# Optimization experiments

Hardware: AMD Instinct MI355X
Metric: run time of the kernel (lower is better)

## Reference

```python
import jax, jax.numpy as jnp
import numpy as np

B, S, E, H = 4, 8192, 1024, 16
D = E // H  # head_dim = 64


def setup_inputs() -> dict:
    key = jax.random.key(0)
    ks = jax.random.split(key, 9)
    s = 0.02
    return {
        "x": jax.random.normal(ks[0], (B, S, E), dtype=jnp.float32),
        "Wq": jax.random.normal(ks[1], (D, E), dtype=jnp.float32) * s,
        "bq": jax.random.normal(ks[2], (D,), dtype=jnp.float32) * s,
        "Wk": jax.random.normal(ks[3], (D, E), dtype=jnp.float32) * s,
        "bk": jax.random.normal(ks[4], (D,), dtype=jnp.float32) * s,
        "Wv": jax.random.normal(ks[5], (D, E), dtype=jnp.float32) * s,
        "bv": jax.random.normal(ks[6], (D,), dtype=jnp.float32) * s,
        "Wo": jax.random.normal(ks[7], (E, E), dtype=jnp.float32) * s,
        "bo": jax.random.normal(ks[8], (E,), dtype=jnp.float32) * s,
    }


def reference(x, Wq, bq, Wk, bk, Wv, bv, Wo, bo):
    b, s, e = x.shape
    d = Wq.shape[0]          # head_dim (projections map embed_dim -> head_dim)
    h = e // d               # num_heads
    # torch Linear: y = x @ W.T + b ; projected shape [B, S, d]
    # view(B, -1, h, d) on [B, S, d] => effective seq S' = S // h (faithful to source)
    def split_heads(t):
        return t.reshape(b, -1, h, d).transpose(0, 2, 1, 3)  # [B, H, S', D]
    q = split_heads(x @ Wq.T + bq)
    k = split_heads(x @ Wk.T + bk)
    v = split_heads(x @ Wv.T + bv)
    scores = jnp.einsum('bhqd,bhkd->bhqk', q, k) / np.sqrt(d).astype(jnp.float32)
    attn = jax.nn.softmax(scores, axis=-1)  # dropout=0.0 => identity
    ctx = jnp.einsum('bhqk,bhkd->bhqd', attn, v)
    ctx = ctx.transpose(0, 2, 1, 3).reshape(b, -1, e)  # [B, S', E]
    return ctx @ Wo.T + bo
```

## Files before the change

### kernel.cpp

```cpp
#include <hip/hip_runtime.h>
#include <hip/hip_bf16.h>


typedef unsigned short u16;
typedef __attribute__((ext_vector_type(8))) short short8;
typedef __attribute__((ext_vector_type(4))) float f32x4;

__device__ inline u16 f2bf(float f) {
    union { float f; unsigned u; } v; v.f = f;
    unsigned u = v.u;
    return (u16)((u + 0x7fffu + ((u >> 16) & 1u)) >> 16);
}
__device__ inline unsigned pack_bf2(float a, float b) {
    union { __hip_bfloat162 h; unsigned u; } v;
    v.h = __float22bfloat162_rn(float2{a, b});
    return v.u;
}
__device__ __forceinline__ void gld16(void* lds, const void* gptr) {
    __builtin_amdgcn_global_load_lds(
        (const __attribute__((address_space(1))) unsigned int*)gptr,
        (__attribute__((address_space(3))) unsigned int*)lds,
        16, 0, 0);
}

__global__ __launch_bounds__(256) void convw(
    const float* __restrict__ Wq, const float* __restrict__ bq,
    const float* __restrict__ Wk, const float* __restrict__ bk,
    const float* __restrict__ Wv, const float* __restrict__ bv,
    const float* __restrict__ Wo,
    u16* __restrict__ Wqkv, float* __restrict__ qkvb, u16* __restrict__ Wob)
{
    const int idx = blockIdx.x * 256 + threadIdx.x;
    Wob[idx] = f2bf(Wo[idx]);
    if (idx < 196608) {
        const int row = idx >> 10, k = idx & 1023;
        float v = (row < 64)  ? Wq[row * 1024 + k] * 0.125f
                : (row < 128) ? Wk[(row - 64) * 1024 + k]
                              : Wv[(row - 128) * 1024 + k];
        Wqkv[idx] = f2bf(v);
    }
    if (idx < 192) {
        qkvb[idx] = (idx < 64) ? bq[idx] * 0.125f
                  : (idx < 128) ? bk[idx - 64] : bv[idx - 128];
    }
}

__global__ __launch_bounds__(256) void qkv_gemm(
    const float* __restrict__ X, const u16* __restrict__ W,
    const float* __restrict__ bias, u16* __restrict__ Out)
{
    __shared__ short8 Bs[2][768];

    const int tid = threadIdx.x;
    const int lane = tid & 63, wid = tid >> 6;
    const int q = lane >> 4, r = lane & 15;
    const long m0 = (long)blockIdx.x * 64;

    const u16* wp[3];
    #pragma unroll
    for (int i = 0; i < 3; ++i)
        wp[i] = W + (long)((wid * 3 + i) * 16 + r) * 1024 + q * 8;

    const float* px = X + (m0 + wid * 16 + r) * 1024 + q * 8;

    f32x4 acc[12] = {};

    #pragma unroll
    for (int i = 0; i < 3; ++i)
        gld16(&Bs[0][wid * 192 + i * 64], wp[i]);
    float4 a0 = *(const float4*)(px);
    float4 a1 = *(const float4*)(px + 4);
    __syncthreads();

    for (int k0 = 0; k0 < 1024; k0 += 32) {
        const int buf = (k0 >> 5) & 1;
        float4 a0n = {}, a1n = {};
        if (k0 + 32 < 1024) {
            #pragma unroll
            for (int i = 0; i < 3; ++i)
                gld16(&Bs[buf ^ 1][wid * 192 + i * 64], wp[i] + k0 + 32);
            a0n = *(const float4*)(px + k0 + 32);
            a1n = *(const float4*)(px + k0 + 36);
        }
        union { short8 s; unsigned u[4]; } af;
        af.u[0] = pack_bf2(a0.x, a0.y);
        af.u[1] = pack_bf2(a0.z, a0.w);
        af.u[2] = pack_bf2(a1.x, a1.y);
        af.u[3] = pack_bf2(a1.z, a1.w);
        #pragma unroll
        for (int nt = 0; nt < 12; ++nt)
            acc[nt] = __builtin_amdgcn_mfma_f32_16x16x32_bf16(
                af.s, Bs[buf][nt * 64 + lane], acc[nt], 0, 0, 0);
        __syncthreads();
        a0 = a0n; a1 = a1n;
    }

    #pragma unroll
    for (int nt = 0; nt < 12; ++nt) {
        const int col = nt * 16 + r;
        const float badd = bias[col];
        #pragma unroll
        for (int e = 0; e < 4; ++e) {
            const long row = m0 + wid * 16 + q * 4 + e;
            Out[row * 192 + col] = f2bf(acc[nt][e] + badd);
        }
    }
}

__global__ __launch_bounds__(256) void vtrans(
    const u16* __restrict__ qkv, u16* __restrict__ Vt)
{
    __shared__ u16 T[64][68];
    const int bh = blockIdx.x, b = bh >> 4, h = bh & 15;
    const int i0 = blockIdx.y * 64;
    const int tid = threadIdx.x;

    #pragma unroll
    for (int it = 0; it < 2; ++it) {
        const int c = tid + 256 * it;
        const int il = c >> 3, d8 = (c & 7) * 8;
        short8 v = *(const short8*)(qkv +
            ((long)b * 8192 + (long)(i0 + il) * 16 + h) * 192 + 128 + d8);
        #pragma unroll
        for (int j = 0; j < 8; ++j) T[d8 + j][il] = (u16)v[j];
    }
    __syncthreads();
    #pragma unroll
    for (int it = 0; it < 2; ++it) {
        const int c = tid + 256 * it;
        const int dl = c >> 3, i8 = (c & 7) * 8;
        short8 o;
        #pragma unroll
        for (int j = 0; j < 8; ++j) o[j] = (short)T[dl][i8 + j];
        *(short8*)(Vt + ((long)bh * 64 + dl) * 512 + i0 + i8) = o;
    }
}

__global__ __launch_bounds__(256) void attn_flash(
    const u16* __restrict__ qkv, const u16* __restrict__ Vt,
    u16* __restrict__ ctx)
{
    __shared__ short8 Ks[2][512];
    __shared__ short8 Vs[2][512];
    __shared__ u16 Plds[4][16 * 72];

    const int tid = threadIdx.x, lane = tid & 63, wid = tid >> 6;
    const int q = lane >> 4, r = lane & 15;
    const int qt = blockIdx.x;
    const int bh = blockIdx.y;
    const int b = bh >> 4, h = bh & 15;
    const long qrowbase = (long)b * 8192 + h;

    short8 Qf0, Qf1;
    {
        const int i = qt * 64 + wid * 16 + r;
        const u16* p = qkv + (qrowbase + (long)i * 16) * 192 + q * 8;
        Qf0 = *(const short8*)(p);
        Qf1 = *(const short8*)(p + 32);
    }

    const u16* kbase = qkv + (qrowbase + (long)(wid * 16 + r) * 16) * 192
                           + 64 + q * 8;
    const u16* vbase = Vt + ((long)bh * 64 + wid * 16 + r) * 512 + q * 8;

    gld16(&Ks[0][wid * 64],       kbase);
    gld16(&Ks[0][256 + wid * 64], kbase + 32);
    gld16(&Vs[0][wid * 64],       vbase);
    gld16(&Vs[0][256 + wid * 64], vbase + 32);
    __syncthreads();

    f32x4 O[4] = {};
    float mrun[4] = {-1e30f, -1e30f, -1e30f, -1e30f};
    float lrun[4] = {};
    u16* Pw = &Plds[wid][0];

    for (int c = 0; c < 8; ++c) {
        const int j0 = c * 64, buf = c & 1;
        if (c < 7) {
            const u16* kp = kbase + (long)(j0 + 64) * 3072;
            const u16* vp = vbase + j0 + 64;
            gld16(&Ks[buf ^ 1][wid * 64],       kp);
            gld16(&Ks[buf ^ 1][256 + wid * 64], kp + 32);
            gld16(&Vs[buf ^ 1][wid * 64],       vp);
            gld16(&Vs[buf ^ 1][256 + wid * 64], vp + 32);
        }
        f32x4 S[4];
        #pragma unroll
        for (int ct = 0; ct < 4; ++ct) {
            f32x4 s = {};
            s = __builtin_amdgcn_mfma_f32_16x16x32_bf16(
                Qf0, Ks[buf][ct * 64 + lane], s, 0, 0, 0);
            s = __builtin_amdgcn_mfma_f32_16x16x32_bf16(
                Qf1, Ks[buf][256 + ct * 64 + lane], s, 0, 0, 0);
            S[ct] = s;
        }
        #pragma unroll
        for (int e = 0; e < 4; ++e) {
            float mc = fmaxf(fmaxf(S[0][e], S[1][e]), fmaxf(S[2][e], S[3][e]));
            #pragma unroll
            for (int off = 1; off < 16; off <<= 1)
                mc = fmaxf(mc, __shfl_xor(mc, off, 64));
            const float mnew = fmaxf(mrun[e], mc);
            const float alpha = __expf(mrun[e] - mnew);
            mrun[e] = mnew;
            float se = 0.f;
            #pragma unroll
            for (int ct = 0; ct < 4; ++ct) {
                const float pv = __expf(S[ct][e] - mnew);
                S[ct][e] = pv; se += pv;
            }
            #pragma unroll
            for (int off = 1; off < 16; off <<= 1)
                se += __shfl_xor(se, off, 64);
            lrun[e] = lrun[e] * alpha + se;
            #pragma unroll
            for (int nt = 0; nt < 4; ++nt) O[nt][e] *= alpha;
        }
        #pragma unroll
        for (int e = 0; e < 4; ++e)
            #pragma unroll
            for (int ct = 0; ct < 4; ++ct)
                Pw[(q * 4 + e) * 72 + ct * 16 + r] = f2bf(S[ct][e]);
        short8 Pf0 = *(const short8*)(Pw + r * 72 + q * 8);
        short8 Pf1 = *(const short8*)(Pw + r * 72 + 32 + q * 8);
        #pragma unroll
        for (int nt = 0; nt < 4; ++nt) {
            O[nt] = __builtin_amdgcn_mfma_f32_16x16x32_bf16(
                Pf0, Vs[buf][nt * 64 + lane], O[nt], 0, 0, 0);
            O[nt] = __builtin_amdgcn_mfma_f32_16x16x32_bf16(
                Pf1, Vs[buf][256 + nt * 64 + lane], O[nt], 0, 0, 0);
        }
        __syncthreads();
    }

    #pragma unroll
    for (int e = 0; e < 4; ++e) {
        const float inv = 1.0f / lrun[e];
        const long i = qt * 64 + wid * 16 + q * 4 + e;
        u16* po = ctx + ((long)b * 512 + i) * 1024 + h * 64 + r;
        #pragma unroll
        for (int nt = 0; nt < 4; ++nt)
            po[nt * 16] = f2bf(O[nt][e] * inv);
    }
}

__global__ __launch_bounds__(256) void gemm_o(
    const u16* __restrict__ A, const u16* __restrict__ B,
    const float* __restrict__ bias, float* __restrict__ C)
{
    __shared__ short8 As[2][512];
    __shared__ short8 Bs[2][512];

    const int tid = threadIdx.x;
    const int lane = tid & 63, wid = tid >> 6;
    const int q = lane >> 4, r = lane & 15;
    const long m0 = (long)blockIdx.x * 64, n0 = (long)blockIdx.y * 64;
    const int wm = wid >> 1, wn = wid & 1;

    const u16* ap[2];
    const u16* bp[2];
    #pragma unroll
    for (int i = 0; i < 2; ++i) {
        const int t = wid * 2 + i, f = t >> 2, mt = t & 3;
        ap[i] = A + (m0 + mt * 16 + r) * 1024 + f * 32 + q * 8;
        bp[i] = B + (n0 + mt * 16 + r) * 1024 + f * 32 + q * 8;
    }

    #pragma unroll
    for (int i = 0; i < 2; ++i) {
        gld16(&As[0][(wid * 2 + i) * 64], ap[i]);
        gld16(&Bs[0][(wid * 2 + i) * 64], bp[i]);
    }
    __syncthreads();

    f32x4 acc[2][2] = {};

    for (int k0 = 0; k0 < 1024; k0 += 64) {
        const int buf = (k0 >> 6) & 1;
        if (k0 + 64 < 1024) {
            #pragma unroll
            for (int i = 0; i < 2; ++i) {
                gld16(&As[buf ^ 1][(wid * 2 + i) * 64], ap[i] + k0 + 64);
                gld16(&Bs[buf ^ 1][(wid * 2 + i) * 64], bp[i] + k0 + 64);
            }
        }
        #pragma unroll
        for (int f = 0; f < 2; ++f) {
            short8 af0 = As[buf][f * 256 + (wm * 2 + 0) * 64 + lane];
            short8 af1 = As[buf][f * 256 + (wm * 2 + 1) * 64 + lane];
            short8 bf0 = Bs[buf][f * 256 + (wn * 2 + 0) * 64 + lane];
            short8 bf1 = Bs[buf][f * 256 + (wn * 2 + 1) * 64 + lane];
            acc[0][0] = __builtin_amdgcn_mfma_f32_16x16x32_bf16(af0, bf0, acc[0][0], 0, 0, 0);
            acc[0][1] = __builtin_amdgcn_mfma_f32_16x16x32_bf16(af0, bf1, acc[0][1], 0, 0, 0);
            acc[1][0] = __builtin_amdgcn_mfma_f32_16x16x32_bf16(af1, bf0, acc[1][0], 0, 0, 0);
            acc[1][1] = __builtin_amdgcn_mfma_f32_16x16x32_bf16(af1, bf1, acc[1][1], 0, 0, 0);
        }
        __syncthreads();
    }

    #pragma unroll
    for (int i = 0; i < 2; ++i)
        #pragma unroll
        for (int j = 0; j < 2; ++j) {
            const long col = n0 + (wn * 2 + j) * 16 + r;
            const float badd = bias[col];
            #pragma unroll
            for (int e = 0; e < 4; ++e) {
                const long row = m0 + (wm * 2 + i) * 16 + q * 4 + e;
                C[row * 1024 + col] = acc[i][j][e] + badd;
            }
        }
}

extern "C" void kernel_launch(void* const* d_in, const int* in_sizes, int n_in,
                              void* d_out, int out_size, void* d_ws, size_t ws_size,
                              hipStream_t stream)
{
    const float* x  = (const float*)d_in[0];
    const float* Wq = (const float*)d_in[1];
    const float* bq = (const float*)d_in[2];
    const float* Wk = (const float*)d_in[3];
    const float* bk = (const float*)d_in[4];
    const float* Wv = (const float*)d_in[5];
    const float* bv = (const float*)d_in[6];
    const float* Wo = (const float*)d_in[7];
    const float* bo = (const float*)d_in[8];
    float* out = (float*)d_out;
    char* ws = (char*)d_ws;

    u16*   qkv  = (u16*)(ws);
    u16*   Vt   = (u16*)(ws + 12582912);
    u16*   Wqkv = (u16*)(ws + 16777216);
    u16*   Wob  = (u16*)(ws + 17170432);
    float* qkvb = (float*)(ws + 19267584);
    u16*   ctx  = (u16*)(ws + 19268352);

    convw<<<4096, 256, 0, stream>>>(Wq, bq, Wk, bk, Wv, bv, Wo, Wqkv, qkvb, Wob);
    qkv_gemm<<<512, 256, 0, stream>>>(x, Wqkv, qkvb, qkv);
    vtrans<<<dim3(64, 8), 256, 0, stream>>>(qkv, Vt);
    attn_flash<<<dim3(8, 64), 256, 0, stream>>>(qkv, Vt, ctx);
    gemm_o<<<dim3(32, 16), 256, 0, stream>>>(ctx, Wob, bo, out);
}
```

Before: 273.8 us.

## Transpose attention MFMA operands and deepen QKV GEMM K-step to 64

The QKV projection GEMM now stages two 32-wide K slices of weights per iteration (double the LDS buffer), halving the loop trip count and barrier count per block. The attention kernel swaps the MFMA operand order so each lane holds one query row's scores across its accumulator elements. That cuts the row max/sum reductions from four 16-lane shuffle trees to two cross-quad shuffles, shrinks the per-row softmax state to a scalar, and enables packed 8-byte stores of P and the output. Costs are more LDS in the GEMM and more in-flight register state.

```diff
diff --git a/kernel.cpp b/kernel.cpp
--- a/kernel.cpp
+++ b/kernel.cpp
@@ -49,50 +49,61 @@
     const float* __restrict__ X, const u16* __restrict__ W,
     const float* __restrict__ bias, u16* __restrict__ Out)
 {
-    __shared__ short8 Bs[2][768];
+    __shared__ short8 Bs[2][1536];
 
     const int tid = threadIdx.x;
     const int lane = tid & 63, wid = tid >> 6;
     const int q = lane >> 4, r = lane & 15;
     const long m0 = (long)blockIdx.x * 64;
 
-    const u16* wp[3];
-    #pragma unroll
-    for (int i = 0; i < 3; ++i)
-        wp[i] = W + (long)((wid * 3 + i) * 16 + r) * 1024 + q * 8;
+    const u16* wp[6];
+    #pragma unroll
+    for (int i = 0; i < 6; ++i) {
+        const int p = wid * 6 + i, kk2 = p / 12, nt = p % 12;
+        wp[i] = W + (long)(nt * 16 + r) * 1024 + kk2 * 32 + q * 8;
+    }
 
     const float* px = X + (m0 + wid * 16 + r) * 1024 + q * 8;
 
     f32x4 acc[12] = {};
 
     #pragma unroll
-    for (int i = 0; i < 3; ++i)
-        gld16(&Bs[0][wid * 192 + i * 64], wp[i]);
-    float4 a0 = *(const float4*)(px);
-    float4 a1 = *(const float4*)(px + 4);
+    for (int i = 0; i < 6; ++i)
+        gld16(&Bs[0][(wid * 6 + i) * 64], wp[i]);
+    float4 a[4];
+    a[0] = *(const float4*)(px);
+    a[1] = *(const float4*)(px + 4);
+    a[2] = *(const float4*)(px + 32);
+    a[3] = *(const float4*)(px + 36);
     __syncthreads();
 
-    for (int k0 = 0; k0 < 1024; k0 += 32) {
-        const int buf = (k0 >> 5) & 1;
-        float4 a0n = {}, a1n = {};
-        if (k0 + 32 < 1024) {
-            #pragma unroll
-            for (int i = 0; i < 3; ++i)
-                gld16(&Bs[buf ^ 1][wid * 192 + i * 64], wp[i] + k0 + 32);
-            a0n = *(const float4*)(px + k0 + 32);
-            a1n = *(const float4*)(px + k0 + 36);
-        }
-        union { short8 s; unsigned u[4]; } af;
-        af.u[0] = pack_bf2(a0.x, a0.y);
-        af.u[1] = pack_bf2(a0.z, a0.w);
-        af.u[2] = pack_bf2(a1.x, a1.y);
-        af.u[3] = pack_bf2(a1.z, a1.w);
-        #pragma unroll
-        for (int nt = 0; nt < 12; ++nt)
-            acc[nt] = __builtin_amdgcn_mfma_f32_16x16x32_bf16(
-                af.s, Bs[buf][nt * 64 + lane], acc[nt], 0, 0, 0);
+    for (int k0 = 0; k0 < 1024; k0 += 64) {
+        const int buf = (k0 >> 6) & 1;
+        float4 an[4] = {};
+        if (k0 + 64 < 1024) {
+            #pragma unroll
+            for (int i = 0; i < 6; ++i)
+                gld16(&Bs[buf ^ 1][(wid * 6 + i) * 64], wp[i] + k0 + 64);
+            an[0] = *(const float4*)(px + k0 + 64);
+            an[1] = *(const float4*)(px + k0 + 68);
+            an[2] = *(const float4*)(px + k0 + 96);
+            an[3] = *(const float4*)(px + k0 + 100);
+        }
+        #pragma unroll
+        for (int kk2 = 0; kk2 < 2; ++kk2) {
+            union { short8 s; unsigned u[4]; } af;
+            af.u[0] = pack_bf2(a[kk2 * 2].x, a[kk2 * 2].y);
+            af.u[1] = pack_bf2(a[kk2 * 2].z, a[kk2 * 2].w);
+            af.u[2] = pack_bf2(a[kk2 * 2 + 1].x, a[kk2 * 2 + 1].y);
+            af.u[3] = pack_bf2(a[kk2 * 2 + 1].z, a[kk2 * 2 + 1].w);
+            #pragma unroll
+            for (int nt = 0; nt < 12; ++nt)
+                acc[nt] = __builtin_amdgcn_mfma_f32_16x16x32_bf16(
+                    af.s, Bs[buf][(kk2 * 12 + nt) * 64 + lane], acc[nt], 0, 0, 0);
+        }
         __syncthreads();
-        a0 = a0n; a1 = a1n;
+        #pragma unroll
+        for (int i = 0; i < 4; ++i) a[i] = an[i];
     }
 
     #pragma unroll
@@ -170,8 +181,7 @@
     __syncthreads();
 
     f32x4 O[4] = {};
-    float mrun[4] = {-1e30f, -1e30f, -1e30f, -1e30f};
-    float lrun[4] = {};
+    float mrun = -1e30f, lrun = 0.f;
     u16* Pw = &Plds[wid][0];
 
     for (int c = 0; c < 8; ++c) {
@@ -189,58 +199,64 @@
         for (int ct = 0; ct < 4; ++ct) {
             f32x4 s = {};
             s = __builtin_amdgcn_mfma_f32_16x16x32_bf16(
-                Qf0, Ks[buf][ct * 64 + lane], s, 0, 0, 0);
+                Ks[buf][ct * 64 + lane], Qf0, s, 0, 0, 0);
             s = __builtin_amdgcn_mfma_f32_16x16x32_bf16(
-                Qf1, Ks[buf][256 + ct * 64 + lane], s, 0, 0, 0);
+                Ks[buf][256 + ct * 64 + lane], Qf1, s, 0, 0, 0);
             S[ct] = s;
         }
-        #pragma unroll
-        for (int e = 0; e < 4; ++e) {
-            float mc = fmaxf(fmaxf(S[0][e], S[1][e]), fmaxf(S[2][e], S[3][e]));
-            #pragma unroll
-            for (int off = 1; off < 16; off <<= 1)
-                mc = fmaxf(mc, __shfl_xor(mc, off, 64));
-            const float mnew = fmaxf(mrun[e], mc);
-            const float alpha = __expf(mrun[e] - mnew);
-            mrun[e] = mnew;
-            float se = 0.f;
-            #pragma unroll
-            for (int ct = 0; ct < 4; ++ct) {
+        float mc = -1e30f;
+        #pragma unroll
+        for (int ct = 0; ct < 4; ++ct)
+            mc = fmaxf(mc, fmaxf(fmaxf(S[ct][0], S[ct][1]),
+                                 fmaxf(S[ct][2], S[ct][3])));
+        mc = fmaxf(mc, __shfl_xor(mc, 16, 64));
+        mc = fmaxf(mc, __shfl_xor(mc, 32, 64));
+        const float mnew = fmaxf(mrun, mc);
+        const float alpha = __expf(mrun - mnew);
+        mrun = mnew;
+        float se = 0.f;
+        #pragma unroll
+        for (int ct = 0; ct < 4; ++ct)
+            #pragma unroll
+            for (int e = 0; e < 4; ++e) {
                 const float pv = __expf(S[ct][e] - mnew);
                 S[ct][e] = pv; se += pv;
             }
-            #pragma unroll
-            for (int off = 1; off < 16; off <<= 1)
-                se += __shfl_xor(se, off, 64);
-            lrun[e] = lrun[e] * alpha + se;
-            #pragma unroll
-            for (int nt = 0; nt < 4; ++nt) O[nt][e] *= alpha;
-        }
-        #pragma unroll
-        for (int e = 0; e < 4; ++e)
-            #pragma unroll
-            for (int ct = 0; ct < 4; ++ct)
-                Pw[(q * 4 + e) * 72 + ct * 16 + r] = f2bf(S[ct][e]);
+        se += __shfl_xor(se, 16, 64);
+        se += __shfl_xor(se, 32, 64);
+        lrun = lrun * alpha + se;
+        #pragma unroll
+        for (int nt = 0; nt < 4; ++nt)
+            #pragma unroll
+            for (int e = 0; e < 4; ++e) O[nt][e] *= alpha;
+        #pragma unroll
+        for (int ct = 0; ct < 4; ++ct) {
+            uint2 d;
+            d.x = pack_bf2(S[ct][0], S[ct][1]);
+            d.y = pack_bf2(S[ct][2], S[ct][3]);
+            *(uint2*)(Pw + r * 72 + ct * 16 + q * 4) = d;
+        }
         short8 Pf0 = *(const short8*)(Pw + r * 72 + q * 8);
         short8 Pf1 = *(const short8*)(Pw + r * 72 + 32 + q * 8);
         #pragma unroll
         for (int nt = 0; nt < 4; ++nt) {
             O[nt] = __builtin_amdgcn_mfma_f32_16x16x32_bf16(
-                Pf0, Vs[buf][nt * 64 + lane], O[nt], 0, 0, 0);
+                Vs[buf][nt * 64 + lane], Pf0, O[nt], 0, 0, 0);
             O[nt] = __builtin_amdgcn_mfma_f32_16x16x32_bf16(
-                Pf1, Vs[buf][256 + nt * 64 + lane], O[nt], 0, 0, 0);
+                Vs[buf][256 + nt * 64 + lane], Pf1, O[nt], 0, 0, 0);
         }
         __syncthreads();
     }
 
-    #pragma unroll
-    for (int e = 0; e < 4; ++e) {
-        const float inv = 1.0f / lrun[e];
-        const long i = qt * 64 + wid * 16 + q * 4 + e;
-        u16* po = ctx + ((long)b * 512 + i) * 1024 + h * 64 + r;
-        #pragma unroll
-        for (int nt = 0; nt < 4; ++nt)
-            po[nt * 16] = f2bf(O[nt][e] * inv);
+    const float inv = 1.0f / lrun;
+    const long i = qt * 64 + wid * 16 + r;
+    u16* po = ctx + ((long)b * 512 + i) * 1024 + h * 64;
+    #pragma unroll
+    for (int nt = 0; nt < 4; ++nt) {
+        uint2 d;
+        d.x = pack_bf2(O[nt][0] * inv, O[nt][1] * inv);
+        d.y = pack_bf2(O[nt][2] * inv, O[nt][3] * inv);
+        *(uint2*)(po + nt * 16 + q * 4) = d;
     }
 }
 
```

Result: faster. 263.8 us (-3.7%).
